# Kernel optimization log

Measured on AMD Instinct MI355X. Metric: run time of the kernel, lower is better.

Reference implementation:

```python
import jax, jax.numpy as jnp
import numpy as np
from jax import lax

# Problem constants (match input_specs): 16 clouds x 4096 points, ratio 0.25
N = 65536
B = 16
N_PER = 4096
RATIO = 0.25
M = int(N_PER * RATIO)  # 1024 sampled points per cloud
D = 512                 # feature dim


def setup_inputs() -> dict:
    key = jax.random.key(0)
    kx, kp = jax.random.split(key)
    x = jax.random.normal(kx, (N, D), dtype=jnp.float32)
    pos = jax.random.normal(kp, (N, 3), dtype=jnp.float32)
    # contiguous equal-sized batches, as produced by a PyG DataLoader with equal cloud sizes
    batch = (jnp.arange(N) // N_PER).astype(jnp.int32)
    return {"x": x, "pos": pos, "batch": batch}


def _fps_one(pos_b):
    """Farthest point sampling on one cloud. pos_b: [N_PER, 3] -> local idx [M] int32.
    Deterministic start at point 0 (torch_cluster.fps with random_start=False)."""
    big = jnp.asarray(1e30, pos_b.dtype)

    def step(carry, _):
        dist, last = carry
        d2 = jnp.sum((pos_b - pos_b[last]) ** 2, axis=-1)  # [N_PER]
        dist = jnp.minimum(dist, d2)
        nxt = jnp.argmax(dist).astype(jnp.int32)
        return (dist, nxt), nxt

    init = (jnp.full((pos_b.shape[0],), big, pos_b.dtype), jnp.int32(0))
    _, rest = lax.scan(step, init, None, length=M - 1)  # [M-1]
    return jnp.concatenate([jnp.zeros((1,), jnp.int32), rest])


def reference(x, pos, batch):
    # per-cloud FPS (batches are contiguous and equal-sized)
    pos_b = pos.reshape(B, N_PER, 3)
    local = jax.vmap(_fps_one)(pos_b)  # [B, M]
    offs = (jnp.arange(B, dtype=jnp.int32) * N_PER)[:, None]
    idx = (local + offs).reshape(-1)   # [B*M] global indices
    # irregular gather of x / pos / batch, as in GraphPool.forward
    return x[idx], pos[idx], batch[idx]
```

## Files before the change

### kernel.cpp

```cpp
#include <hip/hip_runtime.h>

#define N_PER   4096
#define M_SAMP  1024
#define B_CL    16
#define D_FEAT  512
#define TPB     256
#define NWAVE   (TPB / 64)
#define PPT     (N_PER / TPB)
#define NPAIR   (PPT / 2)

typedef float v2f __attribute__((ext_vector_type(2)));

template <int CTRL>
__device__ __forceinline__ unsigned dpp_maxu(unsigned v) {
    unsigned o = (unsigned)__builtin_amdgcn_update_dpp((int)v, (int)v, CTRL, 0xF, 0xF, false);
    return (o > v) ? o : v;
}

__global__ __launch_bounds__(TPB)
__attribute__((amdgpu_waves_per_eu(1, 1)))
void fps_kernel(const float* __restrict__ pos, int* __restrict__ sidx) {
    __shared__ float4             spos[N_PER];
    __shared__ unsigned long long sw[2][NWAVE];
    __shared__ int                sloc[M_SAMP];

    const int cloud = blockIdx.x;
    const int tid   = threadIdx.x;
    const float* posb = pos + (size_t)cloud * N_PER * 3;

    v2f px2[NPAIR], py2[NPAIR], pz2[NPAIR], dist2[NPAIR];
    const int base = tid * PPT;
    {
        float f[48];
        const float4* posb4 = (const float4*)posb + tid * 12;
#pragma unroll
        for (int v = 0; v < 12; ++v) {
            float4 t = posb4[v];
            f[4 * v + 0] = t.x; f[4 * v + 1] = t.y;
            f[4 * v + 2] = t.z; f[4 * v + 3] = t.w;
        }
#pragma unroll
        for (int p = 0; p < NPAIR; ++p) {
            px2[p] = (v2f){f[6 * p + 0], f[6 * p + 3]};
            py2[p] = (v2f){f[6 * p + 1], f[6 * p + 4]};
            pz2[p] = (v2f){f[6 * p + 2], f[6 * p + 5]};
            dist2[p] = (v2f){1e30f, 1e30f};
        }
#pragma unroll
        for (int j = 0; j < PPT; ++j)
            spos[base + j] = make_float4(f[3 * j], f[3 * j + 1], f[3 * j + 2], 0.0f);
    }

    float lx = posb[0], ly = posb[1], lz = posb[2];
    if (tid == 0) sloc[0] = 0;

    const int wave = tid >> 6;
    const int lane = tid & 63;
    __syncthreads();

    for (int s = 1; s < M_SAMP; ++s) {
        float bv = -1.0f;
        v2f lxv = {lx, lx}, lyv = {ly, ly}, lzv = {lz, lz};
#pragma unroll
        for (int p = 0; p < NPAIR; ++p) {
#pragma clang fp contract(off)
            v2f dx = px2[p] - lxv;
            v2f dy = py2[p] - lyv;
            v2f dz = pz2[p] - lzv;
            v2f d2 = dx * dx + dy * dy + dz * dz;
            v2f dn = __builtin_elementwise_min(dist2[p], d2);
            dist2[p] = dn;
            asm("v_max3_f32 %0, %1, %2, %3" : "=v"(bv) : "v"(bv), "v"(dn.x), "v"(dn.y));
        }

        int bj = 0;
#pragma unroll
        for (int j = PPT - 1; j >= 0; --j) {
            float dj = (j & 1) ? dist2[j >> 1].y : dist2[j >> 1].x;
            bj = (dj == bv) ? j : bj;
        }

        unsigned khi = __float_as_uint(bv);
        unsigned r = khi;
        r = dpp_maxu<0xB1>(r);
        r = dpp_maxu<0x4E>(r);
        r = dpp_maxu<0x141>(r);
        r = dpp_maxu<0x140>(r);
        r = dpp_maxu<0x142>(r);
        r = dpp_maxu<0x143>(r);

        unsigned smax = (unsigned)__builtin_amdgcn_readlane((int)r, 63);
        unsigned long long mask = __ballot(khi == smax);
        int sl = __builtin_ctzll(mask);
        int widx_w = __builtin_amdgcn_readlane(base + bj, sl);

        const int buf = s & 1;
        if (lane == 0)
            sw[buf][wave] = ((unsigned long long)smax << 32) |
                            (unsigned)(N_PER - 1 - widx_w);
        __syncthreads();

        unsigned long long k = sw[buf][0];
#pragma unroll
        for (int w = 1; w < NWAVE; ++w) {
            unsigned long long k2 = sw[buf][w];
            if (k2 > k) k = k2;
        }
        int widx = N_PER - 1 - (int)(unsigned)(k & 0xFFFu);
        float4 wp = spos[widx];
        lx = wp.x; ly = wp.y; lz = wp.z;
        if (tid == 0) sloc[s] = widx;
    }

    __syncthreads();
    for (int i = tid; i < M_SAMP; i += TPB)
        sidx[cloud * M_SAMP + i] = sloc[i];
}

__global__ __launch_bounds__(256) void gather_x_kernel(const float4* __restrict__ x4,
                                                       const int* __restrict__ sidx,
                                                       float4* __restrict__ out4) {
    int id = blockIdx.x * 256 + threadIdx.x;
    int r  = id >> 7;
    int c  = id & 127;
    int g  = sidx[r] + (r >> 10 << 12);
    out4[id] = x4[(size_t)g * (D_FEAT / 4) + c];
}

__global__ __launch_bounds__(256) void gather_pb_kernel(const float* __restrict__ pos,
                                                        const int* __restrict__ batch,
                                                        const int* __restrict__ sidx,
                                                        float* __restrict__ out_pos,
                                                        float* __restrict__ out_batch) {
    int r = blockIdx.x * 256 + threadIdx.x;
    int g = sidx[r] + (r >> 10 << 12);
    out_pos[r * 3 + 0] = pos[g * 3 + 0];
    out_pos[r * 3 + 1] = pos[g * 3 + 1];
    out_pos[r * 3 + 2] = pos[g * 3 + 2];
    out_batch[r] = (float)batch[g];
}

extern "C" void kernel_launch(void* const* d_in, const int* in_sizes, int n_in,
                              void* d_out, int out_size, void* d_ws, size_t ws_size,
                              hipStream_t stream) {
    const float* x     = (const float*)d_in[0];
    const float* pos   = (const float*)d_in[1];
    const int*   batch = (const int*)d_in[2];

    int* sidx = (int*)d_ws;

    float* out   = (float*)d_out;
    float* out_x = out;
    float* out_p = out + (size_t)B_CL * M_SAMP * D_FEAT;
    float* out_b = out_p + (size_t)B_CL * M_SAMP * 3;

    fps_kernel<<<B_CL, TPB, 0, stream>>>(pos, sidx);

    gather_x_kernel<<<(B_CL * M_SAMP * (D_FEAT / 4)) / 256, 256, 0, stream>>>(
        (const float4*)x, sidx, (float4*)out_x);

    gather_pb_kernel<<<(B_CL * M_SAMP) / 256, 256, 0, stream>>>(
        pos, batch, sidx, out_p, out_b);
}
```

Before: 729.7 us.

## Process two clouds per FPS block to share barriers across clouds

Each FPS block now handles two point clouds at once, interleaving their distance updates and reductions so that one __syncthreads per step covers both clouds. This halves the number of blocks (8 instead of 16) and doubles per-thread register state and shared memory. The intent is to amortize barrier and reduction latency and expose ILP between independent clouds, at the cost of doing twice the serial work per block on fewer CUs.

```diff
diff --git a/kernel.cpp b/kernel.cpp
--- a/kernel.cpp
+++ b/kernel.cpp
@@ -8,6 +8,7 @@
 #define NWAVE   (TPB / 64)
 #define PPT     (N_PER / TPB)
 #define NPAIR   (PPT / 2)
+#define CPB     2
 
 typedef float v2f __attribute__((ext_vector_type(2)));
 
@@ -20,17 +21,22 @@
 __global__ __launch_bounds__(TPB)
 __attribute__((amdgpu_waves_per_eu(1, 1)))
 void fps_kernel(const float* __restrict__ pos, int* __restrict__ sidx) {
-    __shared__ float4             spos[N_PER];
-    __shared__ unsigned long long sw[2][NWAVE];
-    __shared__ int                sloc[M_SAMP];
+    __shared__ float4             spos[CPB][N_PER];
+    __shared__ unsigned long long swk[CPB][2][NWAVE];
+    __shared__ int                sloc[CPB][M_SAMP];
 
-    const int cloud = blockIdx.x;
-    const int tid   = threadIdx.x;
-    const float* posb = pos + (size_t)cloud * N_PER * 3;
+    const int tid  = threadIdx.x;
+    const int wave = tid >> 6;
+    const int lane = tid & 63;
+    const int base = tid * PPT;
 
-    v2f px2[NPAIR], py2[NPAIR], pz2[NPAIR], dist2[NPAIR];
-    const int base = tid * PPT;
-    {
+    v2f px2[CPB][NPAIR], py2[CPB][NPAIR], pz2[CPB][NPAIR], dist2[CPB][NPAIR];
+    float lx[CPB], ly[CPB], lz[CPB];
+
+#pragma unroll
+    for (int c = 0; c < CPB; ++c) {
+        const int cloud = blockIdx.x * CPB + c;
+        const float* posb = pos + (size_t)cloud * N_PER * 3;
         float f[48];
         const float4* posb4 = (const float4*)posb + tid * 12;
 #pragma unroll
@@ -41,80 +47,86 @@
         }
 #pragma unroll
         for (int p = 0; p < NPAIR; ++p) {
-            px2[p] = (v2f){f[6 * p + 0], f[6 * p + 3]};
-            py2[p] = (v2f){f[6 * p + 1], f[6 * p + 4]};
-            pz2[p] = (v2f){f[6 * p + 2], f[6 * p + 5]};
-            dist2[p] = (v2f){1e30f, 1e30f};
+            px2[c][p] = (v2f){f[6 * p + 0], f[6 * p + 3]};
+            py2[c][p] = (v2f){f[6 * p + 1], f[6 * p + 4]};
+            pz2[c][p] = (v2f){f[6 * p + 2], f[6 * p + 5]};
+            dist2[c][p] = (v2f){1e30f, 1e30f};
         }
 #pragma unroll
         for (int j = 0; j < PPT; ++j)
-            spos[base + j] = make_float4(f[3 * j], f[3 * j + 1], f[3 * j + 2], 0.0f);
+            spos[c][base + j] = make_float4(f[3 * j], f[3 * j + 1], f[3 * j + 2], 0.0f);
+        lx[c] = posb[0]; ly[c] = posb[1]; lz[c] = posb[2];
+        if (tid == 0) sloc[c][0] = 0;
     }
-
-    float lx = posb[0], ly = posb[1], lz = posb[2];
-    if (tid == 0) sloc[0] = 0;
-
-    const int wave = tid >> 6;
-    const int lane = tid & 63;
     __syncthreads();
 
     for (int s = 1; s < M_SAMP; ++s) {
-        float bv = -1.0f;
-        v2f lxv = {lx, lx}, lyv = {ly, ly}, lzv = {lz, lz};
+        const int buf = s & 1;
+
 #pragma unroll
-        for (int p = 0; p < NPAIR; ++p) {
+        for (int c = 0; c < CPB; ++c) {
+            float bv = -1.0f;
+            v2f lxv = {lx[c], lx[c]}, lyv = {ly[c], ly[c]}, lzv = {lz[c], lz[c]};
+#pragma unroll
+            for (int p = 0; p < NPAIR; ++p) {
 #pragma clang fp contract(off)
-            v2f dx = px2[p] - lxv;
-            v2f dy = py2[p] - lyv;
-            v2f dz = pz2[p] - lzv;
-            v2f d2 = dx * dx + dy * dy + dz * dz;
-            v2f dn = __builtin_elementwise_min(dist2[p], d2);
-            dist2[p] = dn;
-            asm("v_max3_f32 %0, %1, %2, %3" : "=v"(bv) : "v"(bv), "v"(dn.x), "v"(dn.y));
+                v2f dx = px2[c][p] - lxv;
+                v2f dy = py2[c][p] - lyv;
+                v2f dz = pz2[c][p] - lzv;
+                v2f d2 = dx * dx + dy * dy + dz * dz;
+                v2f dn = __builtin_elementwise_min(dist2[c][p], d2);
+                dist2[c][p] = dn;
+                asm("v_max3_f32 %0, %1, %2, %3" : "=v"(bv) : "v"(bv), "v"(dn.x), "v"(dn.y));
+            }
+
+            int bj = 0;
+#pragma unroll
+            for (int j = PPT - 1; j >= 0; --j) {
+                float dj = (j & 1) ? dist2[c][j >> 1].y : dist2[c][j >> 1].x;
+                bj = (dj == bv) ? j : bj;
+            }
+
+            unsigned khi = __float_as_uint(bv);
+            unsigned r = khi;
+            r = dpp_maxu<0xB1>(r);
+            r = dpp_maxu<0x4E>(r);
+            r = dpp_maxu<0x141>(r);
+            r = dpp_maxu<0x140>(r);
+            r = dpp_maxu<0x142>(r);
+            r = dpp_maxu<0x143>(r);
+
+            unsigned smax = (unsigned)__builtin_amdgcn_readlane((int)r, 63);
+            unsigned long long mask = __ballot(khi == smax);
+            int sl = __builtin_ctzll(mask);
+            int widx_w = __builtin_amdgcn_readlane(base + bj, sl);
+
+            if (lane == 0)
+                swk[c][buf][wave] = ((unsigned long long)smax << 32) |
+                                    (unsigned)(N_PER - 1 - widx_w);
         }
 
-        int bj = 0;
-#pragma unroll
-        for (int j = PPT - 1; j >= 0; --j) {
-            float dj = (j & 1) ? dist2[j >> 1].y : dist2[j >> 1].x;
-            bj = (dj == bv) ? j : bj;
-        }
-
-        unsigned khi = __float_as_uint(bv);
-        unsigned r = khi;
-        r = dpp_maxu<0xB1>(r);
-        r = dpp_maxu<0x4E>(r);
-        r = dpp_maxu<0x141>(r);
-        r = dpp_maxu<0x140>(r);
-        r = dpp_maxu<0x142>(r);
-        r = dpp_maxu<0x143>(r);
-
-        unsigned smax = (unsigned)__builtin_amdgcn_readlane((int)r, 63);
-        unsigned long long mask = __ballot(khi == smax);
-        int sl = __builtin_ctzll(mask);
-        int widx_w = __builtin_amdgcn_readlane(base + bj, sl);
-
-        const int buf = s & 1;
-        if (lane == 0)
-            sw[buf][wave] = ((unsigned long long)smax << 32) |
-                            (unsigned)(N_PER - 1 - widx_w);
         __syncthreads();
 
-        unsigned long long k = sw[buf][0];
 #pragma unroll
-        for (int w = 1; w < NWAVE; ++w) {
-            unsigned long long k2 = sw[buf][w];
-            if (k2 > k) k = k2;
+        for (int c = 0; c < CPB; ++c) {
+            unsigned long long k = swk[c][buf][0];
+#pragma unroll
+            for (int w = 1; w < NWAVE; ++w) {
+                unsigned long long k2 = swk[c][buf][w];
+                if (k2 > k) k = k2;
+            }
+            int widx = N_PER - 1 - (int)(unsigned)(k & 0xFFFu);
+            float4 wp = spos[c][widx];
+            lx[c] = wp.x; ly[c] = wp.y; lz[c] = wp.z;
+            if (tid == 0) sloc[c][s] = widx;
         }
-        int widx = N_PER - 1 - (int)(unsigned)(k & 0xFFFu);
-        float4 wp = spos[widx];
-        lx = wp.x; ly = wp.y; lz = wp.z;
-        if (tid == 0) sloc[s] = widx;
     }
 
     __syncthreads();
-    for (int i = tid; i < M_SAMP; i += TPB)
-        sidx[cloud * M_SAMP + i] = sloc[i];
+#pragma unroll
+    for (int c = 0; c < CPB; ++c)
+        for (int i = tid; i < M_SAMP; i += TPB)
+            sidx[(blockIdx.x * CPB + c) * M_SAMP + i] = sloc[c][i];
 }
 
 __global__ __launch_bounds__(256) void gather_x_kernel(const float4* __restrict__ x4,
@@ -154,7 +166,7 @@
     float* out_p = out + (size_t)B_CL * M_SAMP * D_FEAT;
     float* out_b = out_p + (size_t)B_CL * M_SAMP * 3;
 
-    fps_kernel<<<B_CL, TPB, 0, stream>>>(pos, sidx);
+    fps_kernel<<<B_CL / CPB, TPB, 0, stream>>>(pos, sidx);
 
     gather_x_kernel<<<(B_CL * M_SAMP * (D_FEAT / 4)) / 256, 256, 0, stream>>>(
         (const float4*)x, sidx, (float4*)out_x);
```

Measured after the change: 1.159 ms. +58.9%, slower.
